# Optimization experiments

Measured on AMD Instinct MI355X. Metric: run time of the kernel, lower is better.

The kernel has to match this reference:

```python
import jax, jax.numpy as jnp
import numpy as np

B = 2_097_152          # batch of theta samples
POLY_DEG = 127         # QSP polynomial degree -> 128 phases
PI = np.float32(np.pi)


def setup_inputs() -> dict:
    key = jax.random.key(0)
    k1, k2 = jax.random.split(key)
    th = jax.random.uniform(k1, (B, 1), dtype=jnp.float32) * PI
    phis = jax.random.uniform(k2, (POLY_DEG + 1, 1), dtype=jnp.float32) * PI
    return {"th": th, "phis": phis}


def reference(th, phis):
    # th: [B,1] float32, phis: [P+1,1] float32 (learned QSP phases)
    theta = th[:, 0]                      # [B]
    c = jnp.cos(theta)
    s = jnp.sin(theta)
    # expm(i*theta*X) = cos(theta) I + i sin(theta) X  (closed form, no expm)
    wx = jnp.stack(
        [jnp.stack([c + 0j, 1j * s], axis=-1),
         jnp.stack([1j * s, c + 0j], axis=-1)],
        axis=-2,
    ).astype(jnp.complex64)               # [B,2,2]

    phi = phis[:, 0]                      # [P+1]
    e = jnp.exp(1j * phi).astype(jnp.complex64)
    # expm(i*phi*Z) = diag(e^{i phi}, e^{-i phi})
    rz = (jnp.zeros((phi.shape[0], 2, 2), jnp.complex64)
          .at[:, 0, 0].set(e)
          .at[:, 1, 1].set(jnp.conj(e)))  # [P+1,2,2]

    u0 = jnp.broadcast_to(rz[0], (theta.shape[0], 2, 2))  # [B,2,2]

    def step(u, rzk):
        u = jnp.einsum('bij,bjk->bik', u, wx)   # u @ W(x)
        u = jnp.einsum('bij,jk->bik', u, rzk)   # ... @ Rz(phi_k)
        return u, None

    u, _ = jax.lax.scan(step, u0, rz[1:])       # 127 sequential steps
    # convention == 0: (Re[u_00], Im[u_00])
    return (jnp.real(u[:, 0, 0]), jnp.imag(u[:, 0, 0]))
```

## Files before the change

### kernel.cpp

```cpp
#include <hip/hip_runtime.h>


#define NPHI 128

__device__ __forceinline__ float wave_shr1(float x) {
    return __builtin_bit_cast(float,
        __builtin_amdgcn_update_dpp(0, __builtin_bit_cast(int, x),
                                    0x138, 0xf, 0xf, true));
}

__global__ __launch_bounds__(256, 4) void qsp_fused(
    const float* __restrict__ th,
    const float* __restrict__ phis,
    float* __restrict__ out,
    int Bq8)
{
    __shared__ alignas(16) float2 g2[NPHI];
    __shared__ float2 h[NPHI];

    const int tid = threadIdx.x;

    if (tid < 64) {
        const int L = tid;
        float sp, cp;
        __sincosf(phis[L], &sp, &cp);
        h[L] = make_float2(0.5f * cp, 0.5f * sp);
        __sincosf(phis[L + 64], &sp, &cp);
        h[L + 64] = make_float2(0.5f * cp, 0.5f * sp);

        float A0r = 0.f, A0i = 0.f, B0r = 0.f, B0i = 0.f;
        float A1r = 0.f, A1i = 0.f, B1r = 0.f, B1i = 0.f;
        const float2 h0 = h[0];
        if (L == 0) { A0r = 2.f * h0.x; A0i = 2.f * h0.y; }

        #pragma unroll 4
        for (int k = 1; k < NPHI; ++k) {
            const float2 hk = h[k];
            const float hx = hk.x, hy = hk.y;
            const float pAr = wave_shr1(A1r), pAi = wave_shr1(A1i);
            const float pBr = wave_shr1(B1r), pBi = wave_shr1(B1i);
            const float u0r = pAr + pBr, u0i = pAi + pBi;
            const float v0r = A0r - B0r, v0i = A0i - B0i;
            const float sA0r = u0r + v0r, sA0i = u0i + v0i;
            const float sB0r = u0r - v0r, sB0i = u0i - v0i;
            const float u1r = A0r + B0r, u1i = A0i + B0i;
            const float v1r = A1r - B1r, v1i = A1i - B1i;
            const float sA1r = u1r + v1r, sA1i = u1i + v1i;
            const float sB1r = u1r - v1r, sB1i = u1i - v1i;
            A0r = fmaf(hx, sA0r, -hy * sA0i);
            A0i = fmaf(hx, sA0i,  hy * sA0r);
            B0r = fmaf(hx, sB0r,  hy * sB0i);
            B0i = fmaf(hx, sB0i, -hy * sB0r);
            A1r = fmaf(hx, sA1r, -hy * sA1i);
            A1i = fmaf(hx, sA1i,  hy * sA1r);
            B1r = fmaf(hx, sB1r,  hy * sB1i);
            B1i = fmaf(hx, sB1i, -hy * sB1r);
        }
        ((float4*)g2)[L] = make_float4(A0r, A0i, A1r, A1i);
    }

    const int idx = blockIdx.x * blockDim.x + tid;
    const int lidx = (idx < Bq8) ? idx : 0;
    const float4 ta = ((const float4*)th)[2 * lidx];
    const float4 tb = ((const float4*)th)[2 * lidx + 1];
    const float th8[8] = {ta.x, ta.y, ta.z, ta.w, tb.x, tb.y, tb.z, tb.w};

    float zr[8], zi[8];
    #pragma unroll
    for (int e = 0; e < 8; ++e) {
        float s, c;
        __sincosf(2.f * th8[e], &s, &c);
        zr[e] = c; zi[e] = s;
    }

    __syncthreads();

    float ar[8], ai[8];
    #pragma unroll
    for (int e = 0; e < 8; ++e) { ar[e] = 0.f; ai[e] = 0.f; }

    const float4* g4 = (const float4*)g2;
    float4 gp = g4[NPHI / 2 - 1];

    #pragma unroll 4
    for (int jj = NPHI / 2 - 1; jj >= 1; --jj) {
        const float4 gn = g4[jj - 1];
        #pragma unroll
        for (int e = 0; e < 8; ++e) {
            const float nr = fmaf(ar[e], zr[e], fmaf(-ai[e], zi[e], gp.z));
            const float ni = fmaf(ar[e], zi[e], fmaf( ai[e], zr[e], gp.w));
            ar[e] = nr; ai[e] = ni;
        }
        #pragma unroll
        for (int e = 0; e < 8; ++e) {
            const float nr = fmaf(ar[e], zr[e], fmaf(-ai[e], zi[e], gp.x));
            const float ni = fmaf(ar[e], zi[e], fmaf( ai[e], zr[e], gp.y));
            ar[e] = nr; ai[e] = ni;
        }
        gp = gn;
    }
    #pragma unroll
    for (int e = 0; e < 8; ++e) {
        const float nr = fmaf(ar[e], zr[e], fmaf(-ai[e], zi[e], gp.z));
        const float ni = fmaf(ar[e], zi[e], fmaf( ai[e], zr[e], gp.w));
        ar[e] = nr; ai[e] = ni;
    }
    #pragma unroll
    for (int e = 0; e < 8; ++e) {
        const float nr = fmaf(ar[e], zr[e], fmaf(-ai[e], zi[e], gp.x));
        const float ni = fmaf(ar[e], zi[e], fmaf( ai[e], zr[e], gp.y));
        ar[e] = nr; ai[e] = ni;
    }

    float orv[8], oiv[8];
    #pragma unroll
    for (int e = 0; e < 8; ++e) {
        float S, C;
        __sincosf(127.f * th8[e], &S, &C);
        orv[e] = fmaf(ar[e], C,  ai[e] * S);
        oiv[e] = fmaf(ai[e], C, -ar[e] * S);
    }

    if (idx < Bq8) {
        float4* o4 = (float4*)out;
        const int ib = 2 * Bq8;
        o4[2 * idx]          = make_float4(orv[0], orv[1], orv[2], orv[3]);
        o4[2 * idx + 1]      = make_float4(orv[4], orv[5], orv[6], orv[7]);
        o4[ib + 2 * idx]     = make_float4(oiv[0], oiv[1], oiv[2], oiv[3]);
        o4[ib + 2 * idx + 1] = make_float4(oiv[4], oiv[5], oiv[6], oiv[7]);
    }
}

extern "C" void kernel_launch(void* const* d_in, const int* in_sizes, int n_in,
                              void* d_out, int out_size, void* d_ws, size_t ws_size,
                              hipStream_t stream)
{
    const float* th   = (const float*)d_in[0];
    const float* phis = (const float*)d_in[1];
    float* out = (float*)d_out;
    const int B = in_sizes[0];
    const int Bq8 = B >> 3;
    const int block = 256;
    const int grid = (Bq8 + block - 1) / block;
    qsp_fused<<<grid, block, 0, stream>>>(th, phis, out, Bq8);
}
```

Baseline: 87.83 us.

## Split phase-coefficient setup into separate one-wave kernel and halve per-thread work

Moves the polynomial coefficient computation, which every block previously redid in its first wave, into a single 64-thread setup kernel that writes a table to workspace. The main kernel reads that table from global memory with uniform loads instead of shared memory and no longer needs a block barrier. Each thread now processes 4 samples instead of 8, doubling the thread count. This removes redundant per-block work and the barrier stall, at the cost of an extra launch and a serial dependency between the two kernels.

```diff
diff --git a/kernel.cpp b/kernel.cpp
--- a/kernel.cpp
+++ b/kernel.cpp
@@ -9,125 +9,103 @@
                                     0x138, 0xf, 0xf, true));
 }
 
-__global__ __launch_bounds__(256, 4) void qsp_fused(
+__global__ __launch_bounds__(64) void qsp_setup(
+    const float* __restrict__ phis,
+    float4* __restrict__ tab)
+{
+    __shared__ float2 h[NPHI];
+    const int L = threadIdx.x;
+
+    float sp, cp;
+    __sincosf(phis[L], &sp, &cp);
+    h[L] = make_float2(0.5f * cp, 0.5f * sp);
+    __sincosf(phis[L + 64], &sp, &cp);
+    h[L + 64] = make_float2(0.5f * cp, 0.5f * sp);
+    __syncthreads();
+
+    float A0r = 0.f, A0i = 0.f, B0r = 0.f, B0i = 0.f;
+    float A1r = 0.f, A1i = 0.f, B1r = 0.f, B1i = 0.f;
+    const float2 h0 = h[0];
+    if (L == 0) { A0r = 2.f * h0.x; A0i = 2.f * h0.y; }
+
+    #pragma unroll 4
+    for (int k = 1; k < NPHI; ++k) {
+        const float2 hk = h[k];
+        const float hx = hk.x, hy = hk.y;
+        const float pAr = wave_shr1(A1r), pAi = wave_shr1(A1i);
+        const float pBr = wave_shr1(B1r), pBi = wave_shr1(B1i);
+        const float u0r = pAr + pBr, u0i = pAi + pBi;
+        const float v0r = A0r - B0r, v0i = A0i - B0i;
+        const float sA0r = u0r + v0r, sA0i = u0i + v0i;
+        const float sB0r = u0r - v0r, sB0i = u0i - v0i;
+        const float u1r = A0r + B0r, u1i = A0i + B0i;
+        const float v1r = A1r - B1r, v1i = A1i - B1i;
+        const float sA1r = u1r + v1r, sA1i = u1i + v1i;
+        const float sB1r = u1r - v1r, sB1i = u1i - v1i;
+        A0r = fmaf(hx, sA0r, -hy * sA0i);
+        A0i = fmaf(hx, sA0i,  hy * sA0r);
+        B0r = fmaf(hx, sB0r,  hy * sB0i);
+        B0i = fmaf(hx, sB0i, -hy * sB0r);
+        A1r = fmaf(hx, sA1r, -hy * sA1i);
+        A1i = fmaf(hx, sA1i,  hy * sA1r);
+        B1r = fmaf(hx, sB1r,  hy * sB1i);
+        B1i = fmaf(hx, sB1i, -hy * sB1r);
+    }
+    tab[L] = make_float4(A0r, A0i, A1r, A1i);
+}
+
+__global__ __launch_bounds__(256) void qsp_main(
     const float* __restrict__ th,
-    const float* __restrict__ phis,
+    const float4* __restrict__ tab,
     float* __restrict__ out,
-    int Bq8)
+    int Bq)
 {
-    __shared__ alignas(16) float2 g2[NPHI];
-    __shared__ float2 h[NPHI];
+    const int idx = blockIdx.x * blockDim.x + threadIdx.x;
+    const int lidx = (idx < Bq) ? idx : 0;
+    const float4 t4 = ((const float4*)th)[lidx];
+    const float th4[4] = {t4.x, t4.y, t4.z, t4.w};
 
-    const int tid = threadIdx.x;
-
-    if (tid < 64) {
-        const int L = tid;
-        float sp, cp;
-        __sincosf(phis[L], &sp, &cp);
-        h[L] = make_float2(0.5f * cp, 0.5f * sp);
-        __sincosf(phis[L + 64], &sp, &cp);
-        h[L + 64] = make_float2(0.5f * cp, 0.5f * sp);
-
-        float A0r = 0.f, A0i = 0.f, B0r = 0.f, B0i = 0.f;
-        float A1r = 0.f, A1i = 0.f, B1r = 0.f, B1i = 0.f;
-        const float2 h0 = h[0];
-        if (L == 0) { A0r = 2.f * h0.x; A0i = 2.f * h0.y; }
-
-        #pragma unroll 4
-        for (int k = 1; k < NPHI; ++k) {
-            const float2 hk = h[k];
-            const float hx = hk.x, hy = hk.y;
-            const float pAr = wave_shr1(A1r), pAi = wave_shr1(A1i);
-            const float pBr = wave_shr1(B1r), pBi = wave_shr1(B1i);
-            const float u0r = pAr + pBr, u0i = pAi + pBi;
-            const float v0r = A0r - B0r, v0i = A0i - B0i;
-            const float sA0r = u0r + v0r, sA0i = u0i + v0i;
-            const float sB0r = u0r - v0r, sB0i = u0i - v0i;
-            const float u1r = A0r + B0r, u1i = A0i + B0i;
-            const float v1r = A1r - B1r, v1i = A1i - B1i;
-            const float sA1r = u1r + v1r, sA1i = u1i + v1i;
-            const float sB1r = u1r - v1r, sB1i = u1i - v1i;
-            A0r = fmaf(hx, sA0r, -hy * sA0i);
-            A0i = fmaf(hx, sA0i,  hy * sA0r);
-            B0r = fmaf(hx, sB0r,  hy * sB0i);
-            B0i = fmaf(hx, sB0i, -hy * sB0r);
-            A1r = fmaf(hx, sA1r, -hy * sA1i);
-            A1i = fmaf(hx, sA1i,  hy * sA1r);
-            B1r = fmaf(hx, sB1r,  hy * sB1i);
-            B1i = fmaf(hx, sB1i, -hy * sB1r);
-        }
-        ((float4*)g2)[L] = make_float4(A0r, A0i, A1r, A1i);
-    }
-
-    const int idx = blockIdx.x * blockDim.x + tid;
-    const int lidx = (idx < Bq8) ? idx : 0;
-    const float4 ta = ((const float4*)th)[2 * lidx];
-    const float4 tb = ((const float4*)th)[2 * lidx + 1];
-    const float th8[8] = {ta.x, ta.y, ta.z, ta.w, tb.x, tb.y, tb.z, tb.w};
-
-    float zr[8], zi[8];
+    float zr[4], zi[4];
     #pragma unroll
-    for (int e = 0; e < 8; ++e) {
+    for (int e = 0; e < 4; ++e) {
         float s, c;
-        __sincosf(2.f * th8[e], &s, &c);
+        __sincosf(2.f * th4[e], &s, &c);
         zr[e] = c; zi[e] = s;
     }
 
-    __syncthreads();
+    float ar[4] = {0.f, 0.f, 0.f, 0.f};
+    float ai[4] = {0.f, 0.f, 0.f, 0.f};
 
-    float ar[8], ai[8];
-    #pragma unroll
-    for (int e = 0; e < 8; ++e) { ar[e] = 0.f; ai[e] = 0.f; }
-
-    const float4* g4 = (const float4*)g2;
-    float4 gp = g4[NPHI / 2 - 1];
-
-    #pragma unroll 4
-    for (int jj = NPHI / 2 - 1; jj >= 1; --jj) {
-        const float4 gn = g4[jj - 1];
+    #pragma unroll 8
+    for (int jj = NPHI / 2 - 1; jj >= 0; --jj) {
+        const float4 gp = tab[jj];
         #pragma unroll
-        for (int e = 0; e < 8; ++e) {
+        for (int e = 0; e < 4; ++e) {
             const float nr = fmaf(ar[e], zr[e], fmaf(-ai[e], zi[e], gp.z));
             const float ni = fmaf(ar[e], zi[e], fmaf( ai[e], zr[e], gp.w));
             ar[e] = nr; ai[e] = ni;
         }
         #pragma unroll
-        for (int e = 0; e < 8; ++e) {
+        for (int e = 0; e < 4; ++e) {
             const float nr = fmaf(ar[e], zr[e], fmaf(-ai[e], zi[e], gp.x));
             const float ni = fmaf(ar[e], zi[e], fmaf( ai[e], zr[e], gp.y));
             ar[e] = nr; ai[e] = ni;
         }
-        gp = gn;
-    }
-    #pragma unroll
-    for (int e = 0; e < 8; ++e) {
-        const float nr = fmaf(ar[e], zr[e], fmaf(-ai[e], zi[e], gp.z));
-        const float ni = fmaf(ar[e], zi[e], fmaf( ai[e], zr[e], gp.w));
-        ar[e] = nr; ai[e] = ni;
-    }
-    #pragma unroll
-    for (int e = 0; e < 8; ++e) {
-        const float nr = fmaf(ar[e], zr[e], fmaf(-ai[e], zi[e], gp.x));
-        const float ni = fmaf(ar[e], zi[e], fmaf( ai[e], zr[e], gp.y));
-        ar[e] = nr; ai[e] = ni;
     }
 
-    float orv[8], oiv[8];
+    float orv[4], oiv[4];
     #pragma unroll
-    for (int e = 0; e < 8; ++e) {
+    for (int e = 0; e < 4; ++e) {
         float S, C;
-        __sincosf(127.f * th8[e], &S, &C);
+        __sincosf(127.f * th4[e], &S, &C);
         orv[e] = fmaf(ar[e], C,  ai[e] * S);
         oiv[e] = fmaf(ai[e], C, -ar[e] * S);
     }
 
-    if (idx < Bq8) {
+    if (idx < Bq) {
         float4* o4 = (float4*)out;
-        const int ib = 2 * Bq8;
-        o4[2 * idx]          = make_float4(orv[0], orv[1], orv[2], orv[3]);
-        o4[2 * idx + 1]      = make_float4(orv[4], orv[5], orv[6], orv[7]);
-        o4[ib + 2 * idx]     = make_float4(oiv[0], oiv[1], oiv[2], oiv[3]);
-        o4[ib + 2 * idx + 1] = make_float4(oiv[4], oiv[5], oiv[6], oiv[7]);
+        o4[idx]      = make_float4(orv[0], orv[1], orv[2], orv[3]);
+        o4[idx + Bq] = make_float4(oiv[0], oiv[1], oiv[2], oiv[3]);
     }
 }
 
@@ -138,9 +116,13 @@
     const float* th   = (const float*)d_in[0];
     const float* phis = (const float*)d_in[1];
     float* out = (float*)d_out;
+    float4* tab = (float4*)d_ws;
     const int B = in_sizes[0];
-    const int Bq8 = B >> 3;
+    const int Bq = B >> 2;
+
+    qsp_setup<<<1, 64, 0, stream>>>(phis, tab);
+
     const int block = 256;
-    const int grid = (Bq8 + block - 1) / block;
-    qsp_fused<<<grid, block, 0, stream>>>(th, phis, out, Bq8);
+    const int grid = (Bq + block - 1) / block;
+    qsp_main<<<grid, block, 0, stream>>>(th, tab, out, Bq);
 }
```

New measurement: 89.15 us. About the same (+1.5%).
